# Kernel tuning notes

Measured on AMD Instinct MI355X. Metric: run time of the kernel, lower is better.

Reference implementation:

```python
import jax, jax.numpy as jnp
import numpy as np

B, S, IN, E, H, FF, L = 8, 1024, 128, 512, 8, 2048, 4
HD = E // H
EPS = 1e-5


def make_pe(seq_len, d_model):
    position = np.arange(seq_len, dtype=np.float32)[:, None]
    div_term = np.exp(np.arange(0, d_model, 2, dtype=np.float32) * (-np.log(10000.0) / d_model))
    pe = np.zeros((seq_len, d_model), dtype=np.float32)
    pe[:, 0::2] = np.sin(position * div_term)
    pe[:, 1::2] = np.cos(position * div_term)
    return jnp.asarray(pe)


def setup_inputs() -> dict:
    key = jax.random.key(0)
    ks = jax.random.split(key, 16)
    s = 0.02
    return {
        "src": jax.random.normal(ks[0], (B, S, IN), jnp.float32),
        "distances": jax.random.uniform(ks[1], (B, S, S), jnp.float32),
        "proj_w": jax.random.normal(ks[2], (E, IN), jnp.float32) * s,
        "proj_b": jnp.zeros((E,), jnp.float32),
        "bn_g": jnp.ones((E,), jnp.float32),
        "bn_b": jnp.zeros((E,), jnp.float32),
        "in_proj_w": jax.random.normal(ks[3], (3 * E, E), jnp.float32) * s,
        "in_proj_b": jnp.zeros((3 * E,), jnp.float32),
        "dist_scale": jnp.array(1.0, jnp.float32),
        "lin1_w": jax.random.normal(ks[4], (FF, E), jnp.float32) * s,
        "lin1_b": jnp.zeros((FF,), jnp.float32),
        "lin2_w": jax.random.normal(ks[5], (E, FF), jnp.float32) * s,
        "lin2_b": jnp.zeros((E,), jnp.float32),
        "n1_g": jnp.ones((E,), jnp.float32),
        "n1_b": jnp.zeros((E,), jnp.float32),
        "n2_g": jnp.ones((E,), jnp.float32),
        "n2_b": jnp.zeros((E,), jnp.float32),
    }


def layernorm(x, g, b):
    m = jnp.mean(x, axis=-1, keepdims=True)
    v = jnp.var(x, axis=-1, keepdims=True)
    return (x - m) * jax.lax.rsqrt(v + EPS) * g + b


def reference(src, distances, proj_w, proj_b, bn_g, bn_b, in_proj_w, in_proj_b,
              dist_scale, lin1_w, lin1_b, lin2_w, lin2_b, n1_g, n1_b, n2_g, n2_b):
    # input projection
    x = jnp.einsum('bsi,ei->bse', src, proj_w) + proj_b  # [B,S,E]
    # BatchNorm1d over flattened (B*S) dim, training-mode batch stats
    xf = x.reshape(-1, E)
    mu = jnp.mean(xf, axis=0)
    var = jnp.var(xf, axis=0)
    x = ((xf - mu) * jax.lax.rsqrt(var + EPS) * bn_g + bn_b).reshape(B, S, E)
    # positional encoding
    x = x + make_pe(S, E)[None]
    # distance bias (same for every layer)
    dmax = jnp.max(distances, axis=-1, keepdims=True)
    dist_bias = jnp.exp(dist_scale * (1.0 - distances / dmax))  # [B,S,S]
    scale = 1.0 / jnp.sqrt(jnp.float32(HD))
    # num_layers iterations of the SAME (shared-parameter) layer
    for _ in range(L):
        qkv = jnp.einsum('bse,fe->bsf', x, in_proj_w) + in_proj_b  # [B,S,3E]
        q, k, v = jnp.split(qkv, 3, axis=-1)
        q = q.reshape(B, S, H, HD).transpose(0, 2, 1, 3)
        k = k.reshape(B, S, H, HD).transpose(0, 2, 1, 3)
        scores = jnp.einsum('bhqd,bhkd->bhqk', q, k) * scale  # [B,H,S,S]
        attn = jax.nn.softmax(scores, axis=-1)
        avg_w = jnp.mean(attn, axis=1)  # head-averaged weights [B,S,S]
        w = avg_w * dist_bias
        w = w / jnp.sum(w, axis=-1, keepdims=True)
        # NOTE: original bmm uses raw layer input as value (no V/out projection)
        attn_out = jnp.einsum('bqk,bke->bqe', w, x)
        x = layernorm(x + attn_out, n1_g, n1_b)
        ff = jnp.einsum('bsf,ef->bse', jax.nn.relu(jnp.einsum('bse,fe->bsf', x, lin1_w) + lin1_b), lin2_w) + lin2_b
        x = layernorm(x + ff, n2_g, n2_b)
    return x
```

## Files before the change

### kernel.cpp

```cpp
#include <hip/hip_runtime.h>
#include <hip/hip_bf16.h>
#include <math.h>

#define Bz 8
#define Sz 1024
#define INz 128
#define Ez 512
#define Hz 8
#define HDz 64
#define FFz 2048
#define Lz 4
#define Nz (Bz*Sz)
#define EPSf 1e-5f

typedef __attribute__((ext_vector_type(8))) short short8;
typedef __attribute__((ext_vector_type(4))) float floatx4;
#define MFMA16(a,b,c) __builtin_amdgcn_mfma_f32_16x16x32_bf16(a,b,c,0,0,0)

typedef __hip_bfloat16 bf16;

__device__ inline float b2f(bf16 v) { return __bfloat162float(v); }
__device__ inline bf16 f2b(float v) { return __float2bfloat16(v); }

__device__ inline void gload16(const bf16* g, bf16* lds_base)
{
  __builtin_amdgcn_global_load_lds(
      (const __attribute__((address_space(1))) void*)g,
      (__attribute__((address_space(3))) void*)lds_base,
      16, 0, 0);
}

#define FENCE() asm volatile("" ::: "memory")
#define PB() do { FENCE(); __builtin_amdgcn_s_barrier(); FENCE(); } while (0)
#define VMCNT0() asm volatile("s_waitcnt vmcnt(0)" ::: "memory")
#define VMCNT8() asm volatile("s_waitcnt vmcnt(8)" ::: "memory")

__global__ __launch_bounds__(256) void cast_f2b(const float* __restrict__ in,
    bf16* __restrict__ out, int n)
{
  int i = blockIdx.x * 256 + threadIdx.x;
  if (i < n) out[i] = f2b(in[i]);
}

__global__ __launch_bounds__(512, 1) void gemm256(
    const bf16* __restrict__ A, const bf16* __restrict__ Wm,
    const float* __restrict__ bias, bf16* __restrict__ Cb,
    int N, int K, int relu)
{
  int bm = blockIdx.y * 256, bn = blockIdx.x * 256;
  __shared__ __align__(16) bf16 As0[256][64], Bs0[256][64];
  __shared__ __align__(16) bf16 As1[256][64], Bs1[256][64];
  int t = threadIdx.x, wave = t >> 6, lane = t & 63;
  int wm = (wave >> 2) * 128, wn = (wave & 3) * 64;
  int fr = lane & 15, fo = lane >> 4;
  int w8 = wave * 8, lrow = lane >> 3;
  int sc8 = ((lane & 7) ^ (lrow & 7)) * 8;
  floatx4 acc[8][4];
  #pragma unroll
  for (int i = 0; i < 8; ++i)
    #pragma unroll
    for (int j = 0; j < 4; ++j) acc[i][j] = (floatx4){0.f, 0.f, 0.f, 0.f};

  #define STAGE8(DA, DB, kk) do {                                           \
    _Pragma("unroll")                                                        \
    for (int c_ = 0; c_ < 4; ++c_) {                                         \
      int row_ = c_ * 64 + w8 + lrow;                                        \
      gload16(A  + (size_t)(bm + row_) * K + (kk) + sc8, &DA[c_ * 64 + w8][0]);\
      gload16(Wm + (size_t)(bn + row_) * K + (kk) + sc8, &DB[c_ * 64 + w8][0]);\
    } } while (0)

  #define TILE(AA, BB, SA, SB, kk, DOSTAGE) do {                            \
    _Pragma("unroll")                                                        \
    for (int q_ = 0; q_ < 4; ++q_) {                                         \
      short8 a_[4][2], bf_[2][2];                                            \
      _Pragma("unroll")                                                      \
      for (int j_ = 0; j_ < 4; ++j_) {                                       \
        int row_ = wm + ((q_ >> 1) * 4 + j_) * 16 + fr;                      \
        a_[j_][0] = *(const short8*)&AA[row_][((fo) ^ (fr & 7)) * 8];        \
        a_[j_][1] = *(const short8*)&AA[row_][((4 + fo) ^ (fr & 7)) * 8];    \
      }                                                                      \
      _Pragma("unroll")                                                      \
      for (int g_ = 0; g_ < 2; ++g_) {                                       \
        int row_ = wn + ((q_ & 1) * 2 + g_) * 16 + fr;                       \
        bf_[g_][0] = *(const short8*)&BB[row_][((fo) ^ (fr & 7)) * 8];       \
        bf_[g_][1] = *(const short8*)&BB[row_][((4 + fo) ^ (fr & 7)) * 8];   \
      }                                                                      \
      if ((DOSTAGE) && q_ == 0) STAGE8(SA, SB, kk);                          \
      PB();                                                                  \
      __builtin_amdgcn_s_setprio(1);                                         \
      _Pragma("unroll")                                                      \
      for (int j_ = 0; j_ < 4; ++j_)                                         \
        _Pragma("unroll")                                                    \
        for (int g_ = 0; g_ < 2; ++g_) {                                     \
          int fi_ = (q_ >> 1) * 4 + j_, gi_ = (q_ & 1) * 2 + g_;             \
          acc[fi_][gi_] = MFMA16(a_[j_][0], bf_[g_][0], acc[fi_][gi_]);      \
          acc[fi_][gi_] = MFMA16(a_[j_][1], bf_[g_][1], acc[fi_][gi_]);      \
        }                                                                    \
      __builtin_amdgcn_s_setprio(0);                                         \
      if (q_ == 3) VMCNT0();                                                 \
      PB();                                                                  \
    } } while (0)

  int nt = K >> 6;
  STAGE8(As0, Bs0, 0);
  STAGE8(As1, Bs1, 64);
  VMCNT8();
  PB();
  TILE(As0, Bs0, As0, Bs0, 0, 0);
  for (int i = 1; i + 2 < nt; i += 2) {
    TILE(As1, Bs1, As0, Bs0, (i + 1) * 64, 1);
    TILE(As0, Bs0, As1, Bs1, (i + 2) * 64, 1);
  }
  TILE(As1, Bs1, As0, Bs0, 0, 0);
  #undef STAGE8
  #undef TILE

  #pragma unroll
  for (int f = 0; f < 8; ++f) {
    #pragma unroll
    for (int r = 0; r < 4; ++r) {
      int row = bm + wm + f * 16 + (lane >> 4) * 4 + r;
      #pragma unroll
      for (int g = 0; g < 4; ++g) {
        int col = bn + wn + g * 16 + fr;
        float v = acc[f][g][r] + (bias ? bias[col] : 0.f);
        if (relu) v = fmaxf(v, 0.f);
        Cb[(size_t)row * N + col] = f2b(v);
      }
    }
  }
}

__global__ __launch_bounds__(256) void gemm_bt(
    const bf16* __restrict__ A, const bf16* __restrict__ Wm,
    const float* __restrict__ bias, float* __restrict__ Cf,
    bf16* __restrict__ Cb, const float* __restrict__ rowscale,
    int M, int N, int K, long sA, long sW, long sC, int relu)
{
  int z = blockIdx.z;
  A  += (size_t)z * sA;
  Wm += (size_t)z * sW;
  if (rowscale) rowscale += (size_t)z * M;
  size_t cbase = (size_t)z * sC;
  int bm = blockIdx.y * 128, bn = blockIdx.x * 128;
  __shared__ __align__(16) bf16 As0[128][64], Bs0[128][64];
  __shared__ __align__(16) bf16 As1[128][64], Bs1[128][64];
  int t = threadIdx.x, wave = t >> 6, lane = t & 63;
  int wm = (wave >> 1) * 64, wn = (wave & 1) * 64;
  int fr = lane & 15, fo = lane >> 4;
  int srow = lane >> 3;
  int scol = ((lane & 7) ^ srow) * 8;
  floatx4 acc[4][4];
  #pragma unroll
  for (int i = 0; i < 4; ++i)
    #pragma unroll
    for (int j = 0; j < 4; ++j) acc[i][j] = (floatx4){0.f, 0.f, 0.f, 0.f};

  #define STAGE(Ad, Bd, kk) do {                                            \
    _Pragma("unroll")                                                        \
    for (int i_ = 0; i_ < 4; ++i_) {                                         \
      int chunk_ = wave * 4 + i_;                                            \
      int row_ = chunk_ * 8 + srow;                                          \
      gload16(A  + (size_t)(bm + row_) * K + (kk) + scol, &Ad[chunk_ * 8][0]);\
      gload16(Wm + (size_t)(bn + row_) * K + (kk) + scol, &Bd[chunk_ * 8][0]);\
    } } while (0)

  #define COMPUTE(Ad, Bd) do {                                               \
    _Pragma("unroll")                                                        \
    for (int ks_ = 0; ks_ < 2; ++ks_) {                                      \
      int sw_ = ((ks_ * 4 + fo) ^ (fr & 7)) * 8;                             \
      short8 af_[4], bf_[4];                                                 \
      _Pragma("unroll")                                                      \
      for (int rt_ = 0; rt_ < 4; ++rt_)                                      \
        af_[rt_] = *(const short8*)&Ad[wm + rt_ * 16 + fr][sw_];             \
      _Pragma("unroll")                                                      \
      for (int ct_ = 0; ct_ < 4; ++ct_)                                      \
        bf_[ct_] = *(const short8*)&Bd[wn + ct_ * 16 + fr][sw_];             \
      _Pragma("unroll")                                                      \
      for (int rt_ = 0; rt_ < 4; ++rt_)                                      \
        _Pragma("unroll")                                                    \
        for (int ct_ = 0; ct_ < 4; ++ct_)                                    \
          acc[rt_][ct_] = MFMA16(af_[rt_], bf_[ct_], acc[rt_][ct_]);         \
    } } while (0)

  STAGE(As0, Bs0, 0);
  __syncthreads();
  for (int k0 = 0; k0 < K; k0 += 128) {
    if (k0 + 64 < K) STAGE(As1, Bs1, k0 + 64);
    COMPUTE(As0, Bs0);
    __syncthreads();
    if (k0 + 64 < K) {
      if (k0 + 128 < K) STAGE(As0, Bs0, k0 + 128);
      COMPUTE(As1, Bs1);
      __syncthreads();
    }
  }
  #undef STAGE
  #undef COMPUTE

  #pragma unroll
  for (int rt = 0; rt < 4; ++rt) {
    #pragma unroll
    for (int r = 0; r < 4; ++r) {
      int row = bm + wm + rt * 16 + (lane >> 4) * 4 + r;
      float rs = rowscale ? (1.f / rowscale[row]) : 1.f;
      #pragma unroll
      for (int ct = 0; ct < 4; ++ct) {
        int col = bn + wn + ct * 16 + fr;
        float v = acc[rt][ct][r] + (bias ? bias[col] : 0.f);
        if (relu) v = fmaxf(v, 0.f);
        v *= rs;
        if (Cf) Cf[cbase + (size_t)row * N + col] = v;
        if (Cb) Cb[cbase + (size_t)row * N + col] = f2b(v);
      }
    }
  }
}

__global__ __launch_bounds__(256) void bn_stats(const float* __restrict__ x, float* __restrict__ st)
{
  int c = blockIdx.x;
  float s = 0.f, q = 0.f;
  for (int r = threadIdx.x; r < Nz; r += 256) {
    float v = x[(size_t)r * Ez + c];
    s += v; q += v * v;
  }
  for (int o = 32; o; o >>= 1) { s += __shfl_down(s, o); q += __shfl_down(q, o); }
  __shared__ float shs[4], shq[4];
  int w = threadIdx.x >> 6;
  if ((threadIdx.x & 63) == 0) { shs[w] = s; shq[w] = q; }
  __syncthreads();
  if (threadIdx.x == 0) {
    s = shs[0] + shs[1] + shs[2] + shs[3];
    q = shq[0] + shq[1] + shq[2] + shq[3];
    float mu = s / (float)Nz;
    float var = q / (float)Nz - mu * mu;
    st[c] = mu;
    st[Ez + c] = rsqrtf(var + EPSf);
  }
}

__global__ __launch_bounds__(256) void bn_apply_pe(const float* __restrict__ x0,
    const float* __restrict__ st, const float* __restrict__ g,
    const float* __restrict__ b, float* __restrict__ x, bf16* __restrict__ xb)
{
  int idx = blockIdx.x * 256 + threadIdx.x;
  int c = idx & (Ez - 1);
  int r = idx >> 9;
  int s = r & (Sz - 1);
  float dt = expf((float)(c & ~1) * (-9.210340371976184f / (float)Ez));
  float ang = (float)s * dt;
  float pe = (c & 1) ? cosf(ang) : sinf(ang);
  float mu = st[c], rs = st[Ez + c];
  float v = (x0[idx] - mu) * rs * g[c] + b[c] + pe;
  x[idx] = v;
  xb[idx] = f2b(v);
}

__global__ __launch_bounds__(256) void dist_bias_k(const float* __restrict__ dist,
    const float* __restrict__ dsc, bf16* __restrict__ db)
{
  size_t base = (size_t)blockIdx.x * Sz;
  float m = -1e30f;
  for (int j = threadIdx.x; j < Sz; j += 256) m = fmaxf(m, dist[base + j]);
  for (int o = 32; o; o >>= 1) m = fmaxf(m, __shfl_down(m, o));
  __shared__ float sh[4];
  if ((threadIdx.x & 63) == 0) sh[threadIdx.x >> 6] = m;
  __syncthreads();
  m = fmaxf(fmaxf(sh[0], sh[1]), fmaxf(sh[2], sh[3]));
  float sc = dsc[0];
  float inv = 1.f / m;
  for (int j = threadIdx.x; j < Sz; j += 256)
    db[base + j] = f2b(expf(sc * (1.f - dist[base + j] * inv)));
}

__global__ __launch_bounds__(256) void transpose_xb(const bf16* __restrict__ xb,
    bf16* __restrict__ xT)
{
  int b = blockIdx.z, e0 = blockIdx.y * 32, s0 = blockIdx.x * 32;
  __shared__ bf16 T[32][40];
  int t = threadIdx.x, row = t >> 3, c = t & 7;
  *(ushort4*)&T[row][c * 4] = *(const ushort4*)(xb + (size_t)(b * Sz + s0 + row) * Ez + e0 + c * 4);
  __syncthreads();
  ushort4 v;
  unsigned short* vp = (unsigned short*)&v;
  #pragma unroll
  for (int i = 0; i < 4; ++i) vp[i] = *(const unsigned short*)&T[c * 4 + i][row];
  *(ushort4*)(xT + ((size_t)b * Ez + e0 + row) * Sz + s0 + c * 4) = v;
}

__global__ __launch_bounds__(256) void attn_stats2(const bf16* __restrict__ qk,
    float* __restrict__ stats)
{
  int qt = blockIdx.x, h = blockIdx.y, b = blockIdx.z;
  int q0 = qt * 64;
  __shared__ bf16 Qs[64][72];
  __shared__ bf16 Ks[128][72];
  int t = threadIdx.x, wave = t >> 6, lane = t & 63;
  int fr = lane & 15, fo = (lane >> 4) * 8;
  #pragma unroll
  for (int i = 0; i < 2; ++i) {
    int idx = i * 256 + t, row = idx >> 3, c4 = idx & 7;
    *(float4*)&Qs[row][c4 * 8] =
      *(const float4*)(qk + (size_t)(b * Sz + q0 + row) * 1024 + h * 64 + c4 * 8);
  }
  __syncthreads();
  short8 aq0 = *(const short8*)&Qs[wave * 16 + fr][fo];
  short8 aq1 = *(const short8*)&Qs[wave * 16 + fr][32 + fo];
  float m_run[4] = {-1e30f, -1e30f, -1e30f, -1e30f};
  float z_run[4] = {0.f, 0.f, 0.f, 0.f};
  for (int k0 = 0; k0 < Sz; k0 += 128) {
    __syncthreads();
    #pragma unroll
    for (int i = 0; i < 4; ++i) {
      int idx = i * 256 + t, row = idx >> 3, c4 = idx & 7;
      *(float4*)&Ks[row][c4 * 8] =
        *(const float4*)(qk + (size_t)(b * Sz + k0 + row) * 1024 + 512 + h * 64 + c4 * 8);
    }
    __syncthreads();
    float sc[8][4];
    #pragma unroll
    for (int j = 0; j < 8; ++j) {
      floatx4 a4 = (floatx4){0.f, 0.f, 0.f, 0.f};
      short8 b0 = *(const short8*)&Ks[j * 16 + fr][fo];
      short8 b1 = *(const short8*)&Ks[j * 16 + fr][32 + fo];
      a4 = MFMA16(aq0, b0, a4);
      a4 = MFMA16(aq1, b1, a4);
      #pragma unroll
      for (int r = 0; r < 4; ++r) sc[j][r] = a4[r] * 0.125f;
    }
    #pragma unroll
    for (int r = 0; r < 4; ++r) {
      float vm = sc[0][r];
      #pragma unroll
      for (int j = 1; j < 8; ++j) vm = fmaxf(vm, sc[j][r]);
      #pragma unroll
      for (int o = 1; o < 16; o <<= 1) vm = fmaxf(vm, __shfl_xor(vm, o, 16));
      float mn = fmaxf(m_run[r], vm);
      float zb = 0.f;
      #pragma unroll
      for (int j = 0; j < 8; ++j) zb += __expf(sc[j][r] - mn);
      #pragma unroll
      for (int o = 1; o < 16; o <<= 1) zb += __shfl_xor(zb, o, 16);
      z_run[r] = z_run[r] * __expf(m_run[r] - mn) + zb;
      m_run[r] = mn;
    }
  }
  if (fr == 0) {
    int qb = q0 + wave * 16 + (lane >> 4) * 4;
    #pragma unroll
    for (int r = 0; r < 4; ++r) {
      size_t o = ((size_t)(b * Hz + h) * Sz + qb + r) * 2;
      stats[o] = m_run[r];
      stats[o + 1] = z_run[r];
    }
  }
}

__global__ __launch_bounds__(256) void scores_bias(const bf16* __restrict__ qk,
    const bf16* __restrict__ db, const float* __restrict__ stats,
    bf16* __restrict__ aw)
{
  int kt = blockIdx.x, qt = blockIdx.y, b = blockIdx.z;
  int q0 = qt * 128, k0 = kt * 128;
  __shared__ bf16 Qs[128][72];
  __shared__ bf16 Ks[128][72];
  __shared__ float mS[128][9];
  __shared__ float ziS[128][9];
  int t = threadIdx.x, wave = t >> 6, lane = t & 63;
  int fr = lane & 15, fo = (lane >> 4) * 8;
  int wm = (wave >> 1) * 64, wn = (wave & 1) * 64;

  #pragma unroll
  for (int i = 0; i < 4; ++i) {
    int lin = i * 256 + t, h = lin >> 7, q = lin & 127;
    const float* sp = stats + ((size_t)(b * Hz + h) * Sz + q0 + q) * 2;
    mS[q][h] = sp[0];
    ziS[q][h] = 1.f / sp[1];
  }

  floatx4 pac[4][4];
  #pragma unroll
  for (int i = 0; i < 4; ++i)
    #pragma unroll
    for (int j = 0; j < 4; ++j) pac[i][j] = (floatx4){0.f, 0.f, 0.f, 0.f};

  for (int h = 0; h < 8; ++h) {
    __syncthreads();
    #pragma unroll
    for (int i = 0; i < 4; ++i) {
      int idx = i * 256 + t, row = idx >> 3, c4 = idx & 7;
      *(float4*)&Qs[row][c4 * 8] =
        *(const float4*)(qk + (size_t)(b * Sz + q0 + row) * 1024 + h * 64 + c4 * 8);
      *(float4*)&Ks[row][c4 * 8] =
        *(const float4*)(qk + (size_t)(b * Sz + k0 + row) * 1024 + 512 + h * 64 + c4 * 8);
    }
    __syncthreads();
    short8 bfv0[4], bfv1[4];
    #pragma unroll
    for (int ct = 0; ct < 4; ++ct) {
      bfv0[ct] = *(const short8*)&Ks[wn + ct * 16 + fr][fo];
      bfv1[ct] = *(const short8*)&Ks[wn + ct * 16 + fr][32 + fo];
    }
    #pragma unroll
    for (int rt = 0; rt < 4; ++rt) {
      short8 af0 = *(const short8*)&Qs[wm + rt * 16 + fr][fo];
      short8 af1 = *(const short8*)&Qs[wm + rt * 16 + fr][32 + fo];
      floatx4 sc[4];
      #pragma unroll
      for (int ct = 0; ct < 4; ++ct) {
        floatx4 z4 = (floatx4){0.f, 0.f, 0.f, 0.f};
        z4 = MFMA16(af0, bfv0[ct], z4);
        sc[ct] = MFMA16(af1, bfv1[ct], z4);
      }
      #pragma unroll
      for (int r = 0; r < 4; ++r) {
        int qloc = wm + rt * 16 + (lane >> 4) * 4 + r;
        float m = mS[qloc][h], zi = ziS[qloc][h];
        #pragma unroll
        for (int ct = 0; ct < 4; ++ct)
          pac[rt][ct][r] += __expf(sc[ct][r] * 0.125f - m) * zi;
      }
    }
  }

  #pragma unroll
  for (int rt = 0; rt < 4; ++rt) {
    #pragma unroll
    for (int r = 0; r < 4; ++r) {
      int qloc = wm + rt * 16 + (lane >> 4) * 4 + r;
      size_t rowoff = (size_t)(b * Sz + q0 + qloc) * Sz + k0;
      #pragma unroll
      for (int ct = 0; ct < 4; ++ct) {
        int kloc = wn + ct * 16 + fr;
        float p = pac[rt][ct][r] * 0.125f * b2f(db[rowoff + kloc]);
        aw[rowoff + kloc] = f2b(p);
      }
    }
  }
}

__global__ __launch_bounds__(256) void rowsum(const bf16* __restrict__ aw,
    float* __restrict__ den)
{
  size_t base = (size_t)blockIdx.x * Sz;
  int t = threadIdx.x;
  ushort4 u = *(const ushort4*)(aw + base + t * 4);
  float s = __uint_as_float((unsigned)u.x << 16) + __uint_as_float((unsigned)u.y << 16)
          + __uint_as_float((unsigned)u.z << 16) + __uint_as_float((unsigned)u.w << 16);
  for (int o = 32; o; o >>= 1) s += __shfl_down(s, o);
  __shared__ float sh[4];
  if ((t & 63) == 0) sh[t >> 6] = s;
  __syncthreads();
  if (t == 0) den[blockIdx.x] = sh[0] + sh[1] + sh[2] + sh[3];
}

__global__ __launch_bounds__(256) void add_ln(const float* __restrict__ xin,
    const float* __restrict__ dly, const float* __restrict__ g,
    const float* __restrict__ bb, float* __restrict__ xout, bf16* __restrict__ xbout)
{
  size_t base = (size_t)blockIdx.x * Ez;
  int t = threadIdx.x;
  float a0 = xin[base + t] + dly[base + t];
  float a1 = xin[base + t + 256] + dly[base + t + 256];
  float s = a0 + a1, q = a0 * a0 + a1 * a1;
  for (int o = 32; o; o >>= 1) { s += __shfl_down(s, o); q += __shfl_down(q, o); }
  __shared__ float shs[4], shq[4];
  if ((t & 63) == 0) { shs[t >> 6] = s; shq[t >> 6] = q; }
  __syncthreads();
  s = shs[0] + shs[1] + shs[2] + shs[3];
  q = shq[0] + shq[1] + shq[2] + shq[3];
  float mu = s * (1.f / Ez);
  float var = q * (1.f / Ez) - mu * mu;
  float rs = rsqrtf(var + EPSf);
  float v0 = (a0 - mu) * rs * g[t] + bb[t];
  float v1 = (a1 - mu) * rs * g[t + 256] + bb[t + 256];
  xout[base + t] = v0;
  xout[base + t + 256] = v1;
  xbout[base + t] = f2b(v0);
  xbout[base + t + 256] = f2b(v1);
}

extern "C" void kernel_launch(void* const* d_in, const int* in_sizes, int n_in,
                              void* d_out, int out_size, void* d_ws, size_t ws_size,
                              hipStream_t stream)
{
  const float* src        = (const float*)d_in[0];
  const float* distances  = (const float*)d_in[1];
  const float* proj_w     = (const float*)d_in[2];
  const float* proj_b     = (const float*)d_in[3];
  const float* bn_g       = (const float*)d_in[4];
  const float* bn_b       = (const float*)d_in[5];
  const float* in_proj_w  = (const float*)d_in[6];
  const float* in_proj_b  = (const float*)d_in[7];
  const float* dist_scale = (const float*)d_in[8];
  const float* lin1_w     = (const float*)d_in[9];
  const float* lin1_b     = (const float*)d_in[10];
  const float* lin2_w     = (const float*)d_in[11];
  const float* lin2_b     = (const float*)d_in[12];
  const float* n1_g       = (const float*)d_in[13];
  const float* n1_b       = (const float*)d_in[14];
  const float* n2_g       = (const float*)d_in[15];
  const float* n2_b       = (const float*)d_in[16];

  float* x = (float*)d_out;

  float* stats = (float*)d_ws;
  float* den   = stats + 131072;
  float* bnst  = den + 8192;
  float* aout  = bnst + 1024;
  float* x0    = aout;
  bf16* db_b = (bf16*)(aout + (size_t)Nz * Ez);
  bf16* Rqk  = db_b + (size_t)Bz * Sz * Sz;
  bf16* qk   = Rqk;
  bf16* aw   = Rqk + (size_t)Nz * 1024;
  bf16* ff1  = Rqk;
  bf16* xb   = Rqk + (size_t)Nz * FFz;
  bf16* xT   = xb + (size_t)Nz * Ez;
  bf16* srcb = xT + (size_t)Bz * Ez * Sz;
  bf16* wpr  = srcb + (size_t)Nz * INz;
  bf16* wqk  = wpr + Ez * INz;
  bf16* wl1  = wqk + 1024 * Ez;
  bf16* wl2  = wl1 + FFz * Ez;

  cast_f2b<<<(Nz * INz) / 256, 256, 0, stream>>>(src, srcb, Nz * INz);
  cast_f2b<<<(Ez * INz + 255) / 256, 256, 0, stream>>>(proj_w, wpr, Ez * INz);
  cast_f2b<<<(1024 * Ez) / 256, 256, 0, stream>>>(in_proj_w, wqk, 1024 * Ez);
  cast_f2b<<<(FFz * Ez) / 256, 256, 0, stream>>>(lin1_w, wl1, FFz * Ez);
  cast_f2b<<<(Ez * FFz) / 256, 256, 0, stream>>>(lin2_w, wl2, Ez * FFz);

  gemm_bt<<<dim3(Ez / 128, Nz / 128, 1), 256, 0, stream>>>(
      srcb, wpr, proj_b, x0, nullptr, nullptr, Nz, Ez, INz, 0, 0, 0, 0);
  bn_stats<<<Ez, 256, 0, stream>>>(x0, bnst);
  bn_apply_pe<<<(Nz * Ez) / 256, 256, 0, stream>>>(x0, bnst, bn_g, bn_b, x, xb);
  dist_bias_k<<<Bz * Sz, 256, 0, stream>>>(distances, dist_scale, db_b);

  for (int l = 0; l < Lz; ++l) {
    transpose_xb<<<dim3(Sz / 32, Ez / 32, Bz), 256, 0, stream>>>(xb, xT);
    gemm256<<<dim3(1024 / 256, Nz / 256), 512, 0, stream>>>(
        xb, wqk, in_proj_b, qk, 1024, Ez, 0);
    attn_stats2<<<dim3(Sz / 64, Hz, Bz), 256, 0, stream>>>(qk, stats);
    scores_bias<<<dim3(Sz / 128, Sz / 128, Bz), 256, 0, stream>>>(qk, db_b, stats, aw);
    rowsum<<<Bz * Sz, 256, 0, stream>>>(aw, den);
    gemm_bt<<<dim3(Ez / 128, Sz / 128, Bz), 256, 0, stream>>>(
        aw, xT, nullptr, aout, nullptr, den,
        Sz, Ez, Sz, (long)Sz * Sz, (long)Ez * Sz, (long)Sz * Ez, 0);
    add_ln<<<Nz, 256, 0, stream>>>(x, aout, n1_g, n1_b, x, xb);
    gemm256<<<dim3(FFz / 256, Nz / 256), 512, 0, stream>>>(
        xb, wl1, lin1_b, ff1, FFz, Ez, 1);
    gemm_bt<<<dim3(Ez / 128, Nz / 128, 1), 256, 0, stream>>>(
        ff1, wl2, lin2_b, aout, nullptr, nullptr, Nz, Ez, FFz, 0, 0, 0, 0);
    add_ln<<<Nz, 256, 0, stream>>>(x, aout, n2_g, n2_b, x, xb);
  }
}
```

Before: 1.181 ms.

## Fuse attention row sums into scores kernel and remap GEMM workgroups

Drops the separate rowsum kernel. The scores_bias kernel now reduces each row's biased weights across lanes and atomically adds them into den, which attn_stats2 zeroes first. This saves a full re-read of the bf16 attention matrix and one launch per layer, at the cost of atomics and summing fp32 values instead of the rounded bf16 values. It also adds an XCD-aware workgroup remap in gemm256, moves the QK projection from gemm256 to the 128-tile gemm_bt, and vectorises the add_ln loads and stores.

```diff
diff --git a/kernel.cpp b/kernel.cpp
--- a/kernel.cpp
+++ b/kernel.cpp
@@ -47,7 +47,13 @@
     const float* __restrict__ bias, bf16* __restrict__ Cb,
     int N, int K, int relu)
 {
-  int bm = blockIdx.y * 256, bn = blockIdx.x * 256;
+  int gx = gridDim.x, nwg = gx * gridDim.y;
+  int flat = blockIdx.y * gx + blockIdx.x;
+  if (!(nwg & 7)) {
+    int cpx = nwg >> 3;
+    flat = (flat & 7) * cpx + (flat >> 3);
+  }
+  int bm = (flat / gx) * 256, bn = (flat % gx) * 256;
   __shared__ __align__(16) bf16 As0[256][64], Bs0[256][64];
   __shared__ __align__(16) bf16 As1[256][64], Bs1[256][64];
   int t = threadIdx.x, wave = t >> 6, lane = t & 63;
@@ -290,13 +296,14 @@
 }
 
 __global__ __launch_bounds__(256) void attn_stats2(const bf16* __restrict__ qk,
-    float* __restrict__ stats)
+    float* __restrict__ stats, float* __restrict__ den)
 {
   int qt = blockIdx.x, h = blockIdx.y, b = blockIdx.z;
   int q0 = qt * 64;
+  int t = threadIdx.x, wave = t >> 6, lane = t & 63;
+  if (h == 0 && t < 64) den[(size_t)b * Sz + q0 + t] = 0.f;
   __shared__ bf16 Qs[64][72];
   __shared__ bf16 Ks[128][72];
-  int t = threadIdx.x, wave = t >> 6, lane = t & 63;
   int fr = lane & 15, fo = (lane >> 4) * 8;
   #pragma unroll
   for (int i = 0; i < 2; ++i) {
@@ -359,7 +366,7 @@
 
 __global__ __launch_bounds__(256) void scores_bias(const bf16* __restrict__ qk,
     const bf16* __restrict__ db, const float* __restrict__ stats,
-    bf16* __restrict__ aw)
+    bf16* __restrict__ aw, float* __restrict__ den)
 {
   int kt = blockIdx.x, qt = blockIdx.y, b = blockIdx.z;
   int q0 = qt * 128, k0 = kt * 128;
@@ -430,29 +437,19 @@
     for (int r = 0; r < 4; ++r) {
       int qloc = wm + rt * 16 + (lane >> 4) * 4 + r;
       size_t rowoff = (size_t)(b * Sz + q0 + qloc) * Sz + k0;
+      float rsum = 0.f;
       #pragma unroll
       for (int ct = 0; ct < 4; ++ct) {
         int kloc = wn + ct * 16 + fr;
         float p = pac[rt][ct][r] * 0.125f * b2f(db[rowoff + kloc]);
         aw[rowoff + kloc] = f2b(p);
+        rsum += p;
       }
-    }
-  }
-}
-
-__global__ __launch_bounds__(256) void rowsum(const bf16* __restrict__ aw,
-    float* __restrict__ den)
-{
-  size_t base = (size_t)blockIdx.x * Sz;
-  int t = threadIdx.x;
-  ushort4 u = *(const ushort4*)(aw + base + t * 4);
-  float s = __uint_as_float((unsigned)u.x << 16) + __uint_as_float((unsigned)u.y << 16)
-          + __uint_as_float((unsigned)u.z << 16) + __uint_as_float((unsigned)u.w << 16);
-  for (int o = 32; o; o >>= 1) s += __shfl_down(s, o);
-  __shared__ float sh[4];
-  if ((t & 63) == 0) sh[t >> 6] = s;
-  __syncthreads();
-  if (t == 0) den[blockIdx.x] = sh[0] + sh[1] + sh[2] + sh[3];
+      #pragma unroll
+      for (int o = 1; o < 16; o <<= 1) rsum += __shfl_xor(rsum, o, 16);
+      if (fr == 0) atomicAdd(den + (size_t)b * Sz + q0 + qloc, rsum);
+    }
+  }
 }
 
 __global__ __launch_bounds__(256) void add_ln(const float* __restrict__ xin,
@@ -461,8 +458,10 @@
 {
   size_t base = (size_t)blockIdx.x * Ez;
   int t = threadIdx.x;
-  float a0 = xin[base + t] + dly[base + t];
-  float a1 = xin[base + t + 256] + dly[base + t + 256];
+  float2 xi = *(const float2*)(xin + base + t * 2);
+  float2 dl = *(const float2*)(dly + base + t * 2);
+  float a0 = xi.x + dl.x;
+  float a1 = xi.y + dl.y;
   float s = a0 + a1, q = a0 * a0 + a1 * a1;
   for (int o = 32; o; o >>= 1) { s += __shfl_down(s, o); q += __shfl_down(q, o); }
   __shared__ float shs[4], shq[4];
@@ -473,12 +472,15 @@
   float mu = s * (1.f / Ez);
   float var = q * (1.f / Ez) - mu * mu;
   float rs = rsqrtf(var + EPSf);
-  float v0 = (a0 - mu) * rs * g[t] + bb[t];
-  float v1 = (a1 - mu) * rs * g[t + 256] + bb[t + 256];
-  xout[base + t] = v0;
-  xout[base + t + 256] = v1;
-  xbout[base + t] = f2b(v0);
-  xbout[base + t + 256] = f2b(v1);
+  float v0 = (a0 - mu) * rs * g[t * 2] + bb[t * 2];
+  float v1 = (a1 - mu) * rs * g[t * 2 + 1] + bb[t * 2 + 1];
+  float2 vo; vo.x = v0; vo.y = v1;
+  *(float2*)(xout + base + t * 2) = vo;
+  bf16 b0 = f2b(v0), b1 = f2b(v1);
+  ushort2 pk;
+  pk.x = *(unsigned short*)&b0;
+  pk.y = *(unsigned short*)&b1;
+  *(ushort2*)(xbout + base + t * 2) = pk;
 }
 
 extern "C" void kernel_launch(void* const* d_in, const int* in_sizes, int n_in,
@@ -537,11 +539,10 @@
 
   for (int l = 0; l < Lz; ++l) {
     transpose_xb<<<dim3(Sz / 32, Ez / 32, Bz), 256, 0, stream>>>(xb, xT);
-    gemm256<<<dim3(1024 / 256, Nz / 256), 512, 0, stream>>>(
-        xb, wqk, in_proj_b, qk, 1024, Ez, 0);
-    attn_stats2<<<dim3(Sz / 64, Hz, Bz), 256, 0, stream>>>(qk, stats);
-    scores_bias<<<dim3(Sz / 128, Sz / 128, Bz), 256, 0, stream>>>(qk, db_b, stats, aw);
-    rowsum<<<Bz * Sz, 256, 0, stream>>>(aw, den);
+    gemm_bt<<<dim3(1024 / 128, Nz / 128, 1), 256, 0, stream>>>(
+        xb, wqk, in_proj_b, nullptr, qk, nullptr, Nz, 1024, Ez, 0, 0, 0, 0);
+    attn_stats2<<<dim3(Sz / 64, Hz, Bz), 256, 0, stream>>>(qk, stats, den);
+    scores_bias<<<dim3(Sz / 128, Sz / 128, Bz), 256, 0, stream>>>(qk, db_b, stats, aw, den);
     gemm_bt<<<dim3(Ez / 128, Sz / 128, Bz), 256, 0, stream>>>(
         aw, xT, nullptr, aout, nullptr, den,
         Sz, Ez, Sz, (long)Sz * Sz, (long)Ez * Sz, (long)Sz * Ez, 0);
```

Measured after the change: 1.138 ms. -3.7%, faster.
